# Optimization experiments

Hardware: AMD Instinct MI355X
Metric: run time of the kernel (lower is better)

Reference implementation:

```python
import jax, jax.numpy as jnp
import numpy as np

COS_EPS = 1e-8  # torch F.cosine_similarity eps


def setup_inputs() -> dict:
    key = jax.random.key(0)
    k1, k2 = jax.random.split(key)
    N, D = 4096, 1024
    features = jax.random.normal(k1, (N, D), dtype=jnp.float32)
    y = jax.random.randint(k2, (N,), 0, 100, dtype=jnp.int64)
    return {"features": features, "y": y}


def reference(features, y):
    y = y.reshape(-1)
    # shared building blocks: row norms and Gram matrix (one GEMM)
    sq = jnp.sum(features * features, axis=-1)            # [N]
    gram = features @ features.T                           # [N, N]
    # Euclidean cdist via ||a||^2 + ||b||^2 - 2 a.b, safe sqrt (grad 0 at 0)
    d2 = sq[:, None] + sq[None, :] - 2.0 * gram
    pos = d2 > 0
    dist = jnp.where(pos, jnp.sqrt(jnp.where(pos, d2, 1.0)), 0.0)
    # cosine similarity with torch-style eps clamp on norms
    norm = jnp.maximum(jnp.sqrt(sq), COS_EPS)              # [N]
    sim = gram / (norm[:, None] * norm[None, :])
    # (eq - ~eq) = 2*eq - 1 signed mask
    eq = (y[:, None] == y[None, :])
    sgn = jnp.where(eq, 1.0, -1.0).astype(features.dtype)
    # loss = sum(sgn * dist) + sum(-sgn * sim)
    return jnp.sum(sgn * dist) - jnp.sum(sgn * sim)
```

## Files before the change

### kernel.cpp

```cpp
#include <hip/hip_runtime.h>
#include <stdint.h>

typedef __attribute__((ext_vector_type(4)))  int   i32x4;
typedef __attribute__((ext_vector_type(8)))  int   i32x8;
typedef __attribute__((ext_vector_type(16))) float f32x16;

#define NROWS 4096
#define DDIM  1024
#define NKT   16
#define NB    32
#define NBLK  528
#define COS_EPS 1e-8f
#define SCL   0x7F7F7F7F

__device__ __forceinline__ void gload16(const uint8_t* g, uint8_t* l) {
  __builtin_amdgcn_global_load_lds(
      (const __attribute__((address_space(1))) uint32_t*)g,
      (__attribute__((address_space(3))) uint32_t*)l, 16, 0, 0);
}

__device__ __forceinline__ i32x8 cat8(i32x4 lo, i32x4 hi) {
  i32x8 r;
  r[0] = lo[0]; r[1] = lo[1]; r[2] = lo[2]; r[3] = lo[3];
  r[4] = hi[0]; r[5] = hi[1]; r[6] = hi[2]; r[7] = hi[3];
  return r;
}

extern "C" __global__ void __launch_bounds__(256) prep_kernel(
    const float* __restrict__ F, uint8_t* __restrict__ Fb,
    float* __restrict__ sq, float* __restrict__ rn, float* __restrict__ out) {
  if (blockIdx.x == 0 && threadIdx.x == 0) out[0] = 0.f;
  const int row  = blockIdx.x * 4 + (threadIdx.x >> 6);
  const int lane = threadIdx.x & 63;
  const float4* src = (const float4*)(F + (size_t)row * DDIM + lane * 16);
  float4 v[4];
#pragma unroll
  for (int i = 0; i < 4; ++i) v[i] = src[i];
  float s = 0.f;
#pragma unroll
  for (int i = 0; i < 4; ++i)
    s += v[i].x * v[i].x + v[i].y * v[i].y + v[i].z * v[i].z + v[i].w * v[i].w;
  uint32_t d[4];
#pragma unroll
  for (int i = 0; i < 4; ++i) {
    int w = __builtin_amdgcn_cvt_pk_fp8_f32(v[i].x, v[i].y, 0, false);
    w = __builtin_amdgcn_cvt_pk_fp8_f32(v[i].z, v[i].w, w, true);
    d[i] = (uint32_t)w;
  }
  *(uint4*)(Fb + (size_t)row * DDIM + lane * 16) = make_uint4(d[0], d[1], d[2], d[3]);
#pragma unroll
  for (int off = 32; off; off >>= 1) s += __shfl_down(s, off);
  if (lane == 0) {
    sq[row] = s;
    rn[row] = 1.0f / fmaxf(sqrtf(s), COS_EPS);
  }
}

extern "C" __global__ void __launch_bounds__(256, 3) gram_kernel(
    const uint8_t* __restrict__ Fb, const float* __restrict__ sq,
    const float* __restrict__ rn, const int* __restrict__ y,
    float* __restrict__ out) {
  __shared__ __align__(16) uint8_t As[3][8192];
  __shared__ __align__(16) uint8_t Bs[3][8192];
  __shared__ float wsum[4];

  int s = (int)(blockIdx.x & 7) * 66 + (int)(blockIdx.x >> 3);
  int bi = 0, rem0 = s;
  while (rem0 >= NB - bi) { rem0 -= NB - bi; ++bi; }
  const int bj = bi + rem0;
  const bool diag = (bi == bj);

  const int tid  = threadIdx.x;
  const int lane = tid & 63;
  const int wid  = tid >> 6;
  const int wr   = wid >> 1;
  const int wc   = wid & 1;
  const int kg   = lane >> 5;
  const int r32  = lane & 31;

  const int hc   = (tid & 7) ^ ((tid >> 3) & 7);
  const int srow = 2 * (tid >> 3) + ((hc >> 2) & 1);
  const int scol = (hc & 3) * 16;
  const uint8_t* gA = Fb + (size_t)(bi * 128 + srow) * DDIM + scol;
  const uint8_t* gB = Fb + (size_t)(bj * 128 + srow) * DDIM + scol;
  uint8_t* ldsA = &As[0][0] + tid * 16;
  uint8_t* ldsB = &Bs[0][0] + tid * 16;

  int offA[2], offB[2];
#pragma unroll
  for (int mt = 0; mt < 2; ++mt) {
    const int R = wr * 64 + mt * 32 + r32;
    const int u = R >> 1, h = R & 1;
    offA[mt] = u * 128 + (((h << 2) + 2 * kg) ^ (u & 7)) * 16;
  }
#pragma unroll
  for (int nb = 0; nb < 2; ++nb) {
    const int R = wc * 64 + nb * 32 + r32;
    const int u = R >> 1, h = R & 1;
    offB[nb] = u * 128 + (((h << 2) + 2 * kg) ^ (u & 7)) * 16;
  }

  f32x16 acc[2][2] = {};

#define STAGE(kt2) do {                                                     \
    const int _sl = (kt2) % 3;                                              \
    const uint8_t* _a = gA + (kt2) * 64;                                    \
    const uint8_t* _b = gB + (kt2) * 64;                                    \
    gload16(_a,                      ldsA + _sl * 8192);                    \
    gload16(_a + (size_t)64 * DDIM,  ldsA + _sl * 8192 + 4096);             \
    gload16(_b,                      ldsB + _sl * 8192);                    \
    gload16(_b + (size_t)64 * DDIM,  ldsB + _sl * 8192 + 4096);             \
  } while (0)

  STAGE(0); STAGE(1);
  asm volatile("s_waitcnt vmcnt(4)");
  __builtin_amdgcn_s_barrier();
  __builtin_amdgcn_sched_barrier(0);

#pragma unroll 1
  for (int kt = 0; kt < NKT; ++kt) {
    const uint8_t* sa = &As[0][0] + (kt % 3) * 8192;
    const uint8_t* sb = &Bs[0][0] + (kt % 3) * 8192;

    const i32x8 A0 = cat8(*(const i32x4*)(sa + offA[0]),
                          *(const i32x4*)(sa + (offA[0] ^ 16)));
    const i32x8 A1 = cat8(*(const i32x4*)(sa + offA[1]),
                          *(const i32x4*)(sa + (offA[1] ^ 16)));
    const i32x8 B0 = cat8(*(const i32x4*)(sb + offB[0]),
                          *(const i32x4*)(sb + (offB[0] ^ 16)));
    const i32x8 B1 = cat8(*(const i32x4*)(sb + offB[1]),
                          *(const i32x4*)(sb + (offB[1] ^ 16)));

    if (kt + 2 < NKT) STAGE(kt + 2);

    acc[0][0] = __builtin_amdgcn_mfma_scale_f32_32x32x64_f8f6f4(
        A0, B0, acc[0][0], 0, 0, 0, SCL, 0, SCL);
    acc[0][1] = __builtin_amdgcn_mfma_scale_f32_32x32x64_f8f6f4(
        A0, B1, acc[0][1], 0, 0, 0, SCL, 0, SCL);
    acc[1][0] = __builtin_amdgcn_mfma_scale_f32_32x32x64_f8f6f4(
        A1, B0, acc[1][0], 0, 0, 0, SCL, 0, SCL);
    acc[1][1] = __builtin_amdgcn_mfma_scale_f32_32x32x64_f8f6f4(
        A1, B1, acc[1][1], 0, 0, 0, SCL, 0, SCL);

    if (kt + 2 < NKT)       asm volatile("s_waitcnt vmcnt(4)");
    else if (kt == NKT - 2) asm volatile("s_waitcnt vmcnt(0)");
    if (kt < NKT - 1) {
      __builtin_amdgcn_s_barrier();
      __builtin_amdgcn_sched_barrier(0);
    }
  }

#undef STAGE

  float sqc[2], rnc[2];
  int   yc[2];
#pragma unroll
  for (int nb = 0; nb < 2; ++nb) {
    const int gj = bj * 128 + wc * 64 + nb * 32 + r32;
    sqc[nb] = sq[gj]; rnc[nb] = rn[gj]; yc[nb] = y[gj];
  }
  float lsum = 0.f;
#pragma unroll
  for (int mt = 0; mt < 2; ++mt) {
#pragma unroll
    for (int e = 0; e < 16; ++e) {
      const int gi = bi * 128 + wr * 64 + mt * 32 + (e & 3) + 8 * (e >> 2) + 4 * kg;
      const float sqi = sq[gi], rni = rn[gi];
      const int yi = y[gi];
#pragma unroll
      for (int nb = 0; nb < 2; ++nb) {
        const int gj = bj * 128 + wc * 64 + nb * 32 + r32;
        const float g  = acc[mt][nb][e];
        const float d2 = sqi + sqc[nb] - 2.0f * g;
        const float dist = d2 > 0.f ? sqrtf(d2) : 0.f;
        const float sim  = g * rni * rnc[nb];
        const float sgn  = (yi == yc[nb]) ? 1.0f : -1.0f;
        float wgt;
        if (diag) wgt = (gj > gi) ? 2.0f : ((gj == gi) ? 1.0f : 0.0f);
        else      wgt = 2.0f;
        lsum += wgt * sgn * (dist - sim);
      }
    }
  }
#pragma unroll
  for (int off = 32; off; off >>= 1) lsum += __shfl_down(lsum, off);
  if (lane == 0) wsum[wid] = lsum;
  __syncthreads();
  if (tid == 0)
    atomicAdd(out, wsum[0] + wsum[1] + wsum[2] + wsum[3]);
}

extern "C" void kernel_launch(void* const* d_in, const int* in_sizes, int n_in,
                              void* d_out, int out_size, void* d_ws, size_t ws_size,
                              hipStream_t stream) {
  const float* F = (const float*)d_in[0];
  const int*   y = (const int*)d_in[1];
  float* out = (float*)d_out;

  uint8_t* Fb = (uint8_t*)d_ws;
  float*  sq = (float*)((char*)d_ws + (size_t)NROWS * DDIM);
  float*  rn = sq + NROWS;

  prep_kernel<<<NROWS / 4, 256, 0, stream>>>(F, Fb, sq, rn, out);
  gram_kernel<<<NBLK, 256, 0, stream>>>(Fb, sq, rn, y, out);
}
```

Baseline: 35.32 us.

## Use 8 waves per gram block with 64x32 warp tiles

```diff
diff --git a/kernel.cpp b/kernel.cpp
--- a/kernel.cpp
+++ b/kernel.cpp
@@ -56,13 +56,13 @@
   }
 }
 
-extern "C" __global__ void __launch_bounds__(256, 3) gram_kernel(
+extern "C" __global__ void __launch_bounds__(512, 4) gram_kernel(
     const uint8_t* __restrict__ Fb, const float* __restrict__ sq,
     const float* __restrict__ rn, const int* __restrict__ y,
     float* __restrict__ out) {
   __shared__ __align__(16) uint8_t As[3][8192];
   __shared__ __align__(16) uint8_t Bs[3][8192];
-  __shared__ float wsum[4];
+  __shared__ float wsum[8];
 
   int s = (int)(blockIdx.x & 7) * 66 + (int)(blockIdx.x >> 3);
   int bi = 0, rem0 = s;
@@ -73,8 +73,8 @@
   const int tid  = threadIdx.x;
   const int lane = tid & 63;
   const int wid  = tid >> 6;
-  const int wr   = wid >> 1;
-  const int wc   = wid & 1;
+  const int wr   = wid >> 2;
+  const int wc   = wid & 3;
   const int kg   = lane >> 5;
   const int r32  = lane & 31;
 
@@ -86,34 +86,29 @@
   uint8_t* ldsA = &As[0][0] + tid * 16;
   uint8_t* ldsB = &Bs[0][0] + tid * 16;
 
-  int offA[2], offB[2];
+  int offA[2], offB1;
 #pragma unroll
   for (int mt = 0; mt < 2; ++mt) {
     const int R = wr * 64 + mt * 32 + r32;
     const int u = R >> 1, h = R & 1;
     offA[mt] = u * 128 + (((h << 2) + 2 * kg) ^ (u & 7)) * 16;
   }
-#pragma unroll
-  for (int nb = 0; nb < 2; ++nb) {
-    const int R = wc * 64 + nb * 32 + r32;
+  {
+    const int R = wc * 32 + r32;
     const int u = R >> 1, h = R & 1;
-    offB[nb] = u * 128 + (((h << 2) + 2 * kg) ^ (u & 7)) * 16;
+    offB1 = u * 128 + (((h << 2) + 2 * kg) ^ (u & 7)) * 16;
   }
 
-  f32x16 acc[2][2] = {};
+  f32x16 acc[2] = {};
 
 #define STAGE(kt2) do {                                                     \
     const int _sl = (kt2) % 3;                                              \
-    const uint8_t* _a = gA + (kt2) * 64;                                    \
-    const uint8_t* _b = gB + (kt2) * 64;                                    \
-    gload16(_a,                      ldsA + _sl * 8192);                    \
-    gload16(_a + (size_t)64 * DDIM,  ldsA + _sl * 8192 + 4096);             \
-    gload16(_b,                      ldsB + _sl * 8192);                    \
-    gload16(_b + (size_t)64 * DDIM,  ldsB + _sl * 8192 + 4096);             \
+    gload16(gA + (kt2) * 64, ldsA + _sl * 8192);                            \
+    gload16(gB + (kt2) * 64, ldsB + _sl * 8192);                            \
   } while (0)
 
   STAGE(0); STAGE(1);
-  asm volatile("s_waitcnt vmcnt(4)");
+  asm volatile("s_waitcnt vmcnt(2)");
   __builtin_amdgcn_s_barrier();
   __builtin_amdgcn_sched_barrier(0);
 
@@ -126,23 +121,17 @@
                           *(const i32x4*)(sa + (offA[0] ^ 16)));
     const i32x8 A1 = cat8(*(const i32x4*)(sa + offA[1]),
                           *(const i32x4*)(sa + (offA[1] ^ 16)));
-    const i32x8 B0 = cat8(*(const i32x4*)(sb + offB[0]),
-                          *(const i32x4*)(sb + (offB[0] ^ 16)));
-    const i32x8 B1 = cat8(*(const i32x4*)(sb + offB[1]),
-                          *(const i32x4*)(sb + (offB[1] ^ 16)));
+    const i32x8 B0 = cat8(*(const i32x4*)(sb + offB1),
+                          *(const i32x4*)(sb + (offB1 ^ 16)));
 
     if (kt + 2 < NKT) STAGE(kt + 2);
 
-    acc[0][0] = __builtin_amdgcn_mfma_scale_f32_32x32x64_f8f6f4(
-        A0, B0, acc[0][0], 0, 0, 0, SCL, 0, SCL);
-    acc[0][1] = __builtin_amdgcn_mfma_scale_f32_32x32x64_f8f6f4(
-        A0, B1, acc[0][1], 0, 0, 0, SCL, 0, SCL);
-    acc[1][0] = __builtin_amdgcn_mfma_scale_f32_32x32x64_f8f6f4(
-        A1, B0, acc[1][0], 0, 0, 0, SCL, 0, SCL);
-    acc[1][1] = __builtin_amdgcn_mfma_scale_f32_32x32x64_f8f6f4(
-        A1, B1, acc[1][1], 0, 0, 0, SCL, 0, SCL);
+    acc[0] = __builtin_amdgcn_mfma_scale_f32_32x32x64_f8f6f4(
+        A0, B0, acc[0], 0, 0, 0, SCL, 0, SCL);
+    acc[1] = __builtin_amdgcn_mfma_scale_f32_32x32x64_f8f6f4(
+        A1, B0, acc[1], 0, 0, 0, SCL, 0, SCL);
 
-    if (kt + 2 < NKT)       asm volatile("s_waitcnt vmcnt(4)");
+    if (kt + 2 < NKT)       asm volatile("s_waitcnt vmcnt(2)");
     else if (kt == NKT - 2) asm volatile("s_waitcnt vmcnt(0)");
     if (kt < NKT - 1) {
       __builtin_amdgcn_s_barrier();
@@ -152,42 +141,36 @@
 
 #undef STAGE
 
-  float sqc[2], rnc[2];
-  int   yc[2];
-#pragma unroll
-  for (int nb = 0; nb < 2; ++nb) {
-    const int gj = bj * 128 + wc * 64 + nb * 32 + r32;
-    sqc[nb] = sq[gj]; rnc[nb] = rn[gj]; yc[nb] = y[gj];
-  }
+  const int gj = bj * 128 + wc * 32 + r32;
+  const float sqj = sq[gj], rnj = rn[gj];
+  const int yj = y[gj];
   float lsum = 0.f;
 #pragma unroll
   for (int mt = 0; mt < 2; ++mt) {
 #pragma unroll
     for (int e = 0; e < 16; ++e) {
       const int gi = bi * 128 + wr * 64 + mt * 32 + (e & 3) + 8 * (e >> 2) + 4 * kg;
-      const float sqi = sq[gi], rni = rn[gi];
-      const int yi = y[gi];
-#pragma unroll
-      for (int nb = 0; nb < 2; ++nb) {
-        const int gj = bj * 128 + wc * 64 + nb * 32 + r32;
-        const float g  = acc[mt][nb][e];
-        const float d2 = sqi + sqc[nb] - 2.0f * g;
-        const float dist = d2 > 0.f ? sqrtf(d2) : 0.f;
-        const float sim  = g * rni * rnc[nb];
-        const float sgn  = (yi == yc[nb]) ? 1.0f : -1.0f;
-        float wgt;
-        if (diag) wgt = (gj > gi) ? 2.0f : ((gj == gi) ? 1.0f : 0.0f);
-        else      wgt = 2.0f;
-        lsum += wgt * sgn * (dist - sim);
-      }
+      const float g  = acc[mt][e];
+      const float d2 = sq[gi] + sqj - 2.0f * g;
+      const float dist = d2 > 0.f ? sqrtf(d2) : 0.f;
+      const float sim  = g * rn[gi] * rnj;
+      const float sgn  = (y[gi] == yj) ? 1.0f : -1.0f;
+      float wgt;
+      if (diag) wgt = (gj > gi) ? 2.0f : ((gj == gi) ? 1.0f : 0.0f);
+      else      wgt = 2.0f;
+      lsum += wgt * sgn * (dist - sim);
     }
   }
 #pragma unroll
   for (int off = 32; off; off >>= 1) lsum += __shfl_down(lsum, off);
   if (lane == 0) wsum[wid] = lsum;
   __syncthreads();
-  if (tid == 0)
-    atomicAdd(out, wsum[0] + wsum[1] + wsum[2] + wsum[3]);
+  if (tid == 0) {
+    float t = 0.f;
+#pragma unroll
+    for (int i = 0; i < 8; ++i) t += wsum[i];
+    atomicAdd(out, t);
+  }
 }
 
 extern "C" void kernel_launch(void* const* d_in, const int* in_sizes, int n_in,
@@ -202,5 +185,5 @@
   float*  rn = sq + NROWS;
 
   prep_kernel<<<NROWS / 4, 256, 0, stream>>>(F, Fb, sq, rn, out);
-  gram_kernel<<<NBLK, 256, 0, stream>>>(Fb, sq, rn, y, out);
+  gram_kernel<<<NBLK, 512, 0, stream>>>(Fb, sq, rn, y, out);
 }
```

New measurement: 34.16 us (median of 2 runs). 1.03x faster.
